# Kernel tuning notes

Hardware: AMD Instinct MI355X
Metric: run time of the kernel (lower is better)

The kernel has to match this reference:

```python
import jax, jax.numpy as jnp
import numpy as np

B, T, F, H = 2048, 512, 64, 16


def setup_inputs() -> dict:
    key = jax.random.key(0)
    ks = jax.random.split(key, 10)
    s = 0.05  # small init so relu-activated LSTM state stays bounded over 512 steps
    return {
        "x": jax.random.normal(ks[0], (B, T, F), dtype=jnp.float32),
        "Wx": jax.random.normal(ks[1], (F, 4 * H), dtype=jnp.float32) * s,
        "Wh": jax.random.normal(ks[2], (H, 4 * H), dtype=jnp.float32) * s,
        "b": jnp.zeros((4 * H,), dtype=jnp.float32),
        "W2": jax.random.normal(ks[3], (H, 8), dtype=jnp.float32) * 0.3,
        "b2": jnp.zeros((8,), dtype=jnp.float32),
        "W3": jax.random.normal(ks[4], (8, 4), dtype=jnp.float32) * 0.3,
        "b3": jnp.zeros((4,), dtype=jnp.float32),
        "Wo": jax.random.normal(ks[5], (4, 1), dtype=jnp.float32) * 0.3,
        "bo": jnp.zeros((1,), dtype=jnp.float32),
    }


def reference(x, Wx, Wh, b, W2, b2, W3, b3, Wo, bo):
    # Keras LSTM, gate order [i, f, c(g), o]; recurrent_activation=sigmoid,
    # activation=relu (applied to candidate g AND to cell state in h = o*relu(c)).
    # Precompute input projections for all timesteps, scan only the recurrence.
    xz = jnp.einsum('btf,fg->btg', x, Wx) + b  # [B, T, 4H]
    h0 = jnp.zeros((x.shape[0], H), dtype=x.dtype)
    c0 = jnp.zeros((x.shape[0], H), dtype=x.dtype)

    def step(carry, xz_t):
        h, c = carry
        z = xz_t + h @ Wh  # [B, 4H]
        i = jax.nn.sigmoid(z[:, 0 * H:1 * H])
        f = jax.nn.sigmoid(z[:, 1 * H:2 * H])
        g = jax.nn.relu(z[:, 2 * H:3 * H])
        o = jax.nn.sigmoid(z[:, 3 * H:4 * H])
        c_new = f * c + i * g
        h_new = o * jax.nn.relu(c_new)
        return (h_new, c_new), None

    (h_T, _), _ = jax.lax.scan(step, (h0, c0), jnp.swapaxes(xz, 0, 1))
    # Dropout layers are identity at inference (training=False).
    x2 = jax.nn.relu(h_T @ W2 + b2)
    x3 = jax.nn.relu(x2 @ W3 + b3)
    return jax.nn.sigmoid(x3 @ Wo + bo)  # [B, 1]
```

## Files before the change

### kernel.cpp

```cpp
#include <hip/hip_runtime.h>
#include <stdint.h>

#define Bdim 2048
#define Tdim 512
#define NBLK (Tdim / 16)

#define TSTRIDE 68
#define BUFD (16 * TSTRIDE)

typedef __attribute__((ext_vector_type(8))) short bf16x8;
typedef __attribute__((ext_vector_type(4))) float f32x4;

__device__ __forceinline__ uint16_t f2bf(float f) {
    union { float f; uint32_t u; } v; v.f = f;
    uint32_t r = v.u + 0x7fffu + ((v.u >> 16) & 1u);
    return (uint16_t)(r >> 16);
}
__device__ __forceinline__ float sigmoidf(float z) {
    return __builtin_amdgcn_rcpf(1.0f + __expf(-z));
}

__global__ __launch_bounds__(64, 2) void lstm_fused(
    const float* __restrict__ x, const float* __restrict__ Wx,
    const float* __restrict__ bias, const float* __restrict__ Wh,
    const float* __restrict__ W2, const float* __restrict__ b2,
    const float* __restrict__ W3, const float* __restrict__ b3,
    const float* __restrict__ Wo, const float* __restrict__ bo,
    float* __restrict__ out)
{
    __shared__ __align__(16) float zbuf[2 * BUFD];
    __shared__ __align__(16) float hbuf[16];

    const int lane = threadIdx.x;
    const int l15  = lane & 15;
    const int quad = lane >> 4;
    const int b    = blockIdx.x;

    float w[16];
    #pragma unroll
    for (int k = 0; k < 16; ++k) w[k] = Wh[(size_t)k * 64 + lane];

    bf16x8 wxf[4][2];
    #pragma unroll
    for (int nt = 0; nt < 4; ++nt)
        #pragma unroll
        for (int kc = 0; kc < 2; ++kc)
            #pragma unroll
            for (int jj = 0; jj < 8; ++jj)
                wxf[nt][kc][jj] =
                    (short)f2bf(Wx[(size_t)(kc * 32 + quad * 8 + jj) * 64 + nt * 16 + l15]);

    float bv[4];
    #pragma unroll
    for (int nt = 0; nt < 4; ++nt) bv[nt] = bias[nt * 16 + l15];

    float4 xn[4];
    auto load_tile = [&](int t0) {
        const float* p = x + ((size_t)b * Tdim + t0 + l15) * 64 + quad * 8;
        xn[0] = *(const float4*)(p);
        xn[1] = *(const float4*)(p + 4);
        xn[2] = *(const float4*)(p + 32);
        xn[3] = *(const float4*)(p + 36);
    };

    auto project = [&](int q) {
        bf16x8 af[2];
        #pragma unroll
        for (int kc = 0; kc < 2; ++kc) {
            const float4 p0 = xn[kc * 2], p1 = xn[kc * 2 + 1];
            af[kc][0] = (short)f2bf(p0.x); af[kc][1] = (short)f2bf(p0.y);
            af[kc][2] = (short)f2bf(p0.z); af[kc][3] = (short)f2bf(p0.w);
            af[kc][4] = (short)f2bf(p1.x); af[kc][5] = (short)f2bf(p1.y);
            af[kc][6] = (short)f2bf(p1.z); af[kc][7] = (short)f2bf(p1.w);
        }
        f32x4 acc[4];
        #pragma unroll
        for (int nt = 0; nt < 4; ++nt) {
            f32x4 a = {bv[nt], bv[nt], bv[nt], bv[nt]};
            a = __builtin_amdgcn_mfma_f32_16x16x32_bf16(af[0], wxf[nt][0], a, 0, 0, 0);
            a = __builtin_amdgcn_mfma_f32_16x16x32_bf16(af[1], wxf[nt][1], a, 0, 0, 0);
            acc[nt] = a;
        }
        #pragma unroll
        for (int reg = 0; reg < 4; ++reg) {
            float4 w4;
            w4.x = acc[0][reg]; w4.y = acc[1][reg];
            w4.z = acc[2][reg]; w4.w = acc[3][reg];
            *(float4*)&zbuf[q * BUFD + (quad * 4 + reg) * TSTRIDE + l15 * 4] = w4;
        }
    };

    const int zoff = l15 * 4 + quad;
    auto readz = [&](int q, int t) -> float {
        return zbuf[q * BUFD + t * TSTRIDE + zoff];
    };

    load_tile(0);
    project(0);
    load_tile(16);

    float c = 0.f, h = 0.f;
    float hk[16];
    #pragma unroll
    for (int k = 0; k < 16; ++k) hk[k] = 0.f;
    float zc = readz(0, 0);

    for (int n = 0; n < NBLK; ++n) {
        const int p = n & 1;
        if (n + 1 < NBLK) {
            project(p ^ 1);
            if (n + 2 < NBLK) load_tile((n + 2) * 16);
        }
        #pragma unroll
        for (int u = 0; u < 16; ++u) {
            float zn = (u < 15) ? readz(p, u + 1) : readz(p ^ 1, 0);

            float a0 = zc, a1 = 0.f;
            #pragma unroll
            for (int k = 0; k < 8; ++k) {
                a0 = fmaf(hk[k],     w[k],     a0);
                a1 = fmaf(hk[k + 8], w[k + 8], a1);
            }
            const float z = a0 + a1;
            const float sig = sigmoidf(z);
            const float a = (quad == 2) ? fmaxf(z, 0.f) : sig;

            const float i_ = __shfl(a, l15);
            const float f_ = __shfl(a, l15 + 16);
            const float g_ = __shfl(a, l15 + 32);
            const float o_ = __shfl(a, l15 + 48);

            c = fmaf(f_, c, i_ * g_);
            h = o_ * fmaxf(c, 0.f);

            hbuf[l15] = h;
            const float4* hb = (const float4*)hbuf;
            float4 h0 = hb[0], h1 = hb[1], h2 = hb[2], h3 = hb[3];
            hk[0]  = h0.x; hk[1]  = h0.y; hk[2]  = h0.z; hk[3]  = h0.w;
            hk[4]  = h1.x; hk[5]  = h1.y; hk[6]  = h1.z; hk[7]  = h1.w;
            hk[8]  = h2.x; hk[9]  = h2.y; hk[10] = h2.z; hk[11] = h2.w;
            hk[12] = h3.x; hk[13] = h3.y; hk[14] = h3.z; hk[15] = h3.w;

            zc = zn;
        }
    }

    if (lane == 0) {
        float x2[8];
        #pragma unroll
        for (int k = 0; k < 8; ++k) {
            float s = b2[k];
            #pragma unroll
            for (int q = 0; q < 16; ++q) s = fmaf(hk[q], W2[(size_t)q * 8 + k], s);
            x2[k] = fmaxf(s, 0.f);
        }
        float x3[4];
        #pragma unroll
        for (int m = 0; m < 4; ++m) {
            float s = b3[m];
            #pragma unroll
            for (int k = 0; k < 8; ++k) s = fmaf(x2[k], W3[(size_t)k * 4 + m], s);
            x3[m] = fmaxf(s, 0.f);
        }
        float s = bo[0];
        #pragma unroll
        for (int m = 0; m < 4; ++m) s = fmaf(x3[m], Wo[m], s);
        out[b] = sigmoidf(s);
    }
}

extern "C" void kernel_launch(void* const* d_in, const int* in_sizes, int n_in,
                              void* d_out, int out_size, void* d_ws, size_t ws_size,
                              hipStream_t stream) {
    const float* x  = (const float*)d_in[0];
    const float* Wx = (const float*)d_in[1];
    const float* Wh = (const float*)d_in[2];
    const float* bb = (const float*)d_in[3];
    const float* W2 = (const float*)d_in[4];
    const float* b2 = (const float*)d_in[5];
    const float* W3 = (const float*)d_in[6];
    const float* b3 = (const float*)d_in[7];
    const float* Wo = (const float*)d_in[8];
    const float* bo = (const float*)d_in[9];

    lstm_fused<<<Bdim, 64, 0, stream>>>(x, Wx, bb, Wh, W2, b2, W3, b3,
                                        Wo, bo, (float*)d_out);
}
```

Baseline: 386.0 us.

## Batch 16 sequences per block with MFMA recurrence and warp-specialized projection

```diff
diff --git a/kernel.cpp b/kernel.cpp
--- a/kernel.cpp
+++ b/kernel.cpp
@@ -3,13 +3,19 @@
 
 #define Bdim 2048
 #define Tdim 512
-#define NBLK (Tdim / 16)
-
-#define TSTRIDE 68
-#define BUFD (16 * TSTRIDE)
+#define TT 8
+#define NT (Tdim / TT)
+
+#define XSTR (TT * 64 + 4)
+#define XBUF (16 * XSTR)
+#define ZSTR 68
+#define ZTS  (16 * ZSTR)
+#define ZBUF (TT * ZTS)
 
 typedef __attribute__((ext_vector_type(8))) short bf16x8;
 typedef __attribute__((ext_vector_type(4))) float f32x4;
+
+union U32x4 { uint32_t u[4]; bf16x8 v; };
 
 __device__ __forceinline__ uint16_t f2bf(float f) {
     union { float f; uint32_t u; } v; v.f = f;
@@ -19,8 +25,20 @@
 __device__ __forceinline__ float sigmoidf(float z) {
     return __builtin_amdgcn_rcpf(1.0f + __expf(-z));
 }
-
-__global__ __launch_bounds__(64, 2) void lstm_fused(
+__device__ __forceinline__ float fast_exp2(float x) {
+#if __has_builtin(__builtin_amdgcn_exp2f)
+    return __builtin_amdgcn_exp2f(x);
+#else
+    return exp2f(x);
+#endif
+}
+__device__ __forceinline__ void gld16(const float* gsrc, float* ldst) {
+    __builtin_amdgcn_global_load_lds(
+        (__attribute__((address_space(1))) void*)(gsrc),
+        (__attribute__((address_space(3))) void*)(ldst), 16, 0, 0);
+}
+
+__global__ __launch_bounds__(128, 1) void lstm_fused(
     const float* __restrict__ x, const float* __restrict__ Wx,
     const float* __restrict__ bias, const float* __restrict__ Wh,
     const float* __restrict__ W2, const float* __restrict__ b2,
@@ -28,144 +46,170 @@
     const float* __restrict__ Wo, const float* __restrict__ bo,
     float* __restrict__ out)
 {
-    __shared__ __align__(16) float zbuf[2 * BUFD];
-    __shared__ __align__(16) float hbuf[16];
-
-    const int lane = threadIdx.x;
-    const int l15  = lane & 15;
-    const int quad = lane >> 4;
-    const int b    = blockIdx.x;
-
-    float w[16];
-    #pragma unroll
-    for (int k = 0; k < 16; ++k) w[k] = Wh[(size_t)k * 64 + lane];
-
-    bf16x8 wxf[4][2];
-    #pragma unroll
-    for (int nt = 0; nt < 4; ++nt)
-        #pragma unroll
-        for (int kc = 0; kc < 2; ++kc)
-            #pragma unroll
-            for (int jj = 0; jj < 8; ++jj)
-                wxf[nt][kc][jj] =
-                    (short)f2bf(Wx[(size_t)(kc * 32 + quad * 8 + jj) * 64 + nt * 16 + l15]);
-
-    float bv[4];
-    #pragma unroll
-    for (int nt = 0; nt < 4; ++nt) bv[nt] = bias[nt * 16 + l15];
-
-    float4 xn[4];
-    auto load_tile = [&](int t0) {
-        const float* p = x + ((size_t)b * Tdim + t0 + l15) * 64 + quad * 8;
-        xn[0] = *(const float4*)(p);
-        xn[1] = *(const float4*)(p + 4);
-        xn[2] = *(const float4*)(p + 32);
-        xn[3] = *(const float4*)(p + 36);
+    __shared__ __align__(16) float xlds[2 * XBUF];
+    __shared__ __align__(16) float zbuf[2 * ZBUF];
+    __shared__ __align__(16) float hlds[16 * 17];
+
+    const int lane = threadIdx.x & 63;
+    const int wid  = threadIdx.x >> 6;
+    const int q = lane >> 4;
+    const int j = lane & 15;
+    const int b0 = blockIdx.x * 16;
+    const float KLOG2E = 1.4426950408889634f;
+
+    bf16x8 awx[4][2];
+    f32x4  bcol[4];
+    bf16x8 awh[4];
+    float  cst[4] = {0.f, 0.f, 0.f, 0.f};
+    float  hh[4]  = {0.f, 0.f, 0.f, 0.f};
+    uint32_t hw0 = 0, hw1 = 0;
+
+    auto gload = [&](int tile, int buf) {
+        const float* src0 = x + ((size_t)b0 * Tdim + tile * TT) * 64 + lane * 4;
+        #pragma unroll
+        for (int rb = 0; rb < 16; ++rb) {
+            const float* s = src0 + (size_t)rb * Tdim * 64;
+            float* d = &xlds[buf * XBUF + rb * XSTR];
+            gld16(s, d);
+            gld16(s + 256, d + 256);
+        }
     };
 
-    auto project = [&](int q) {
-        bf16x8 af[2];
-        #pragma unroll
-        for (int kc = 0; kc < 2; ++kc) {
-            const float4 p0 = xn[kc * 2], p1 = xn[kc * 2 + 1];
-            af[kc][0] = (short)f2bf(p0.x); af[kc][1] = (short)f2bf(p0.y);
-            af[kc][2] = (short)f2bf(p0.z); af[kc][3] = (short)f2bf(p0.w);
-            af[kc][4] = (short)f2bf(p1.x); af[kc][5] = (short)f2bf(p1.y);
-            af[kc][6] = (short)f2bf(p1.z); af[kc][7] = (short)f2bf(p1.w);
-        }
-        f32x4 acc[4];
+    auto proj = [&](int srcbuf, int dstbuf) {
+        const float* xb = &xlds[srcbuf * XBUF] + j * XSTR + q * 8;
+        float* zb = &zbuf[dstbuf * ZBUF] + j * ZSTR + q * 4;
+        #pragma unroll
+        for (int t = 0; t < TT; ++t) {
+            const float* px = xb + t * 64;
+            f32x4 x0 = *(const f32x4*)(px);
+            f32x4 x1 = *(const f32x4*)(px + 4);
+            f32x4 x2 = *(const f32x4*)(px + 32);
+            f32x4 x3 = *(const f32x4*)(px + 36);
+            U32x4 bx0, bx1;
+            asm("v_cvt_pk_bf16_f32 %0, %1, %2" : "=v"(bx0.u[0]) : "v"(x0[0]), "v"(x0[1]));
+            asm("v_cvt_pk_bf16_f32 %0, %1, %2" : "=v"(bx0.u[1]) : "v"(x0[2]), "v"(x0[3]));
+            asm("v_cvt_pk_bf16_f32 %0, %1, %2" : "=v"(bx0.u[2]) : "v"(x1[0]), "v"(x1[1]));
+            asm("v_cvt_pk_bf16_f32 %0, %1, %2" : "=v"(bx0.u[3]) : "v"(x1[2]), "v"(x1[3]));
+            asm("v_cvt_pk_bf16_f32 %0, %1, %2" : "=v"(bx1.u[0]) : "v"(x2[0]), "v"(x2[1]));
+            asm("v_cvt_pk_bf16_f32 %0, %1, %2" : "=v"(bx1.u[1]) : "v"(x2[2]), "v"(x2[3]));
+            asm("v_cvt_pk_bf16_f32 %0, %1, %2" : "=v"(bx1.u[2]) : "v"(x3[0]), "v"(x3[1]));
+            asm("v_cvt_pk_bf16_f32 %0, %1, %2" : "=v"(bx1.u[3]) : "v"(x3[2]), "v"(x3[3]));
+            #pragma unroll
+            for (int nt = 0; nt < 4; ++nt) {
+                f32x4 a = bcol[nt];
+                a = __builtin_amdgcn_mfma_f32_16x16x32_bf16(awx[nt][0], bx0.v, a, 0, 0, 0);
+                a = __builtin_amdgcn_mfma_f32_16x16x32_bf16(awx[nt][1], bx1.v, a, 0, 0, 0);
+                *(f32x4*)(zb + t * ZTS + nt * 16) = a;
+            }
+        }
+    };
+
+    if (wid == 1) {
         #pragma unroll
         for (int nt = 0; nt < 4; ++nt) {
-            f32x4 a = {bv[nt], bv[nt], bv[nt], bv[nt]};
-            a = __builtin_amdgcn_mfma_f32_16x16x32_bf16(af[0], wxf[nt][0], a, 0, 0, 0);
-            a = __builtin_amdgcn_mfma_f32_16x16x32_bf16(af[1], wxf[nt][1], a, 0, 0, 0);
-            acc[nt] = a;
-        }
-        #pragma unroll
-        for (int reg = 0; reg < 4; ++reg) {
-            float4 w4;
-            w4.x = acc[0][reg]; w4.y = acc[1][reg];
-            w4.z = acc[2][reg]; w4.w = acc[3][reg];
-            *(float4*)&zbuf[q * BUFD + (quad * 4 + reg) * TSTRIDE + l15 * 4] = w4;
-        }
-    };
-
-    const int zoff = l15 * 4 + quad;
-    auto readz = [&](int q, int t) -> float {
-        return zbuf[q * BUFD + t * TSTRIDE + zoff];
-    };
-
-    load_tile(0);
-    project(0);
-    load_tile(16);
-
-    float c = 0.f, h = 0.f;
-    float hk[16];
-    #pragma unroll
-    for (int k = 0; k < 16; ++k) hk[k] = 0.f;
-    float zc = readz(0, 0);
-
-    for (int n = 0; n < NBLK; ++n) {
-        const int p = n & 1;
-        if (n + 1 < NBLK) {
-            project(p ^ 1);
-            if (n + 2 < NBLK) load_tile((n + 2) * 16);
-        }
-        #pragma unroll
-        for (int u = 0; u < 16; ++u) {
-            float zn = (u < 15) ? readz(p, u + 1) : readz(p ^ 1, 0);
-
-            float a0 = zc, a1 = 0.f;
+            const float s = (nt == 2) ? 1.0f : -KLOG2E;
+            #pragma unroll
+            for (int kc = 0; kc < 2; ++kc)
+                #pragma unroll
+                for (int jj = 0; jj < 8; ++jj)
+                    awx[nt][kc][jj] = (short)f2bf(
+                        Wx[(size_t)(kc * 32 + q * 8 + jj) * 64 + nt * 16 + j] * s);
+            #pragma unroll
+            for (int r = 0; r < 4; ++r)
+                bcol[nt][r] = bias[nt * 16 + q * 4 + r] * s;
+        }
+        gload(0, 0);
+        asm volatile("s_waitcnt vmcnt(0)" ::: "memory");
+    } else {
+        #pragma unroll
+        for (int nt = 0; nt < 4; ++nt) {
+            const float s = (nt == 2) ? 1.0f : -KLOG2E;
+            bf16x8 a;
+            #pragma unroll
+            for (int e = 0; e < 8; ++e) a[e] = 0;
+            #pragma unroll
+            for (int e = 0; e < 4; ++e)
+                a[e] = (short)f2bf(Wh[(size_t)(q * 4 + e) * 64 + nt * 16 + j] * s);
+            awh[nt] = a;
+        }
+    }
+    __syncthreads();
+    if (wid == 1) {
+        gload(1, 1);
+        proj(0, 0);
+        asm volatile("s_waitcnt vmcnt(0) lgkmcnt(0)" ::: "memory");
+    }
+    __syncthreads();
+
+    for (int n = 0; n < NT; ++n) {
+        if (wid == 0) {
+            const float* zp = &zbuf[(n & 1) * ZBUF] + j * ZSTR + q * 4;
+            f32x4 zc0 = *(const f32x4*)(zp);
+            f32x4 zc1 = *(const f32x4*)(zp + 16);
+            f32x4 zc2 = *(const f32x4*)(zp + 32);
+            f32x4 zc3 = *(const f32x4*)(zp + 48);
+            #pragma unroll
+            for (int t = 0; t < TT; ++t) {
+                f32x4 zn0, zn1, zn2, zn3;
+                if (t < TT - 1) {
+                    const float* zq = zp + (t + 1) * ZTS;
+                    zn0 = *(const f32x4*)(zq);
+                    zn1 = *(const f32x4*)(zq + 16);
+                    zn2 = *(const f32x4*)(zq + 32);
+                    zn3 = *(const f32x4*)(zq + 48);
+                }
+                U32x4 hbu; hbu.u[0] = hw0; hbu.u[1] = hw1; hbu.u[2] = 0; hbu.u[3] = 0;
+                f32x4 ai = __builtin_amdgcn_mfma_f32_16x16x32_bf16(awh[0], hbu.v, zc0, 0, 0, 0);
+                f32x4 af = __builtin_amdgcn_mfma_f32_16x16x32_bf16(awh[1], hbu.v, zc1, 0, 0, 0);
+                f32x4 ag = __builtin_amdgcn_mfma_f32_16x16x32_bf16(awh[2], hbu.v, zc2, 0, 0, 0);
+                f32x4 ao = __builtin_amdgcn_mfma_f32_16x16x32_bf16(awh[3], hbu.v, zc3, 0, 0, 0);
+                #pragma unroll
+                for (int r = 0; r < 4; ++r) {
+                    float si = __builtin_amdgcn_rcpf(1.0f + fast_exp2(ai[r]));
+                    float sf = __builtin_amdgcn_rcpf(1.0f + fast_exp2(af[r]));
+                    float so = __builtin_amdgcn_rcpf(1.0f + fast_exp2(ao[r]));
+                    float gg = fmaxf(ag[r], 0.0f);
+                    cst[r] = fmaf(sf, cst[r], si * gg);
+                    hh[r] = so * fmaxf(cst[r], 0.0f);
+                }
+                asm("v_cvt_pk_bf16_f32 %0, %1, %2" : "=v"(hw0) : "v"(hh[0]), "v"(hh[1]));
+                asm("v_cvt_pk_bf16_f32 %0, %1, %2" : "=v"(hw1) : "v"(hh[2]), "v"(hh[3]));
+                if (t < TT - 1) { zc0 = zn0; zc1 = zn1; zc2 = zn2; zc3 = zn3; }
+            }
+        } else {
+            if (n + 2 < NT) gload(n + 2, n & 1);
+            if (n + 1 < NT) proj((n + 1) & 1, (n + 1) & 1);
+            asm volatile("s_waitcnt vmcnt(0) lgkmcnt(0)" ::: "memory");
+        }
+        __syncthreads();
+    }
+
+    if (wid == 0) {
+        #pragma unroll
+        for (int r = 0; r < 4; ++r) hlds[j * 17 + q * 4 + r] = hh[r];
+        if (lane < 16) {
+            const float* hp = &hlds[lane * 17];
+            float x2[8];
             #pragma unroll
             for (int k = 0; k < 8; ++k) {
-                a0 = fmaf(hk[k],     w[k],     a0);
-                a1 = fmaf(hk[k + 8], w[k + 8], a1);
-            }
-            const float z = a0 + a1;
-            const float sig = sigmoidf(z);
-            const float a = (quad == 2) ? fmaxf(z, 0.f) : sig;
-
-            const float i_ = __shfl(a, l15);
-            const float f_ = __shfl(a, l15 + 16);
-            const float g_ = __shfl(a, l15 + 32);
-            const float o_ = __shfl(a, l15 + 48);
-
-            c = fmaf(f_, c, i_ * g_);
-            h = o_ * fmaxf(c, 0.f);
-
-            hbuf[l15] = h;
-            const float4* hb = (const float4*)hbuf;
-            float4 h0 = hb[0], h1 = hb[1], h2 = hb[2], h3 = hb[3];
-            hk[0]  = h0.x; hk[1]  = h0.y; hk[2]  = h0.z; hk[3]  = h0.w;
-            hk[4]  = h1.x; hk[5]  = h1.y; hk[6]  = h1.z; hk[7]  = h1.w;
-            hk[8]  = h2.x; hk[9]  = h2.y; hk[10] = h2.z; hk[11] = h2.w;
-            hk[12] = h3.x; hk[13] = h3.y; hk[14] = h3.z; hk[15] = h3.w;
-
-            zc = zn;
-        }
-    }
-
-    if (lane == 0) {
-        float x2[8];
-        #pragma unroll
-        for (int k = 0; k < 8; ++k) {
-            float s = b2[k];
-            #pragma unroll
-            for (int q = 0; q < 16; ++q) s = fmaf(hk[q], W2[(size_t)q * 8 + k], s);
-            x2[k] = fmaxf(s, 0.f);
-        }
-        float x3[4];
-        #pragma unroll
-        for (int m = 0; m < 4; ++m) {
-            float s = b3[m];
-            #pragma unroll
-            for (int k = 0; k < 8; ++k) s = fmaf(x2[k], W3[(size_t)k * 4 + m], s);
-            x3[m] = fmaxf(s, 0.f);
-        }
-        float s = bo[0];
-        #pragma unroll
-        for (int m = 0; m < 4; ++m) s = fmaf(x3[m], Wo[m], s);
-        out[b] = sigmoidf(s);
+                float s = b2[k];
+                #pragma unroll
+                for (int u = 0; u < 16; ++u) s = fmaf(hp[u], W2[(size_t)u * 8 + k], s);
+                x2[k] = fmaxf(s, 0.f);
+            }
+            float x3[4];
+            #pragma unroll
+            for (int m = 0; m < 4; ++m) {
+                float s = b3[m];
+                #pragma unroll
+                for (int k = 0; k < 8; ++k) s = fmaf(x2[k], W3[(size_t)k * 4 + m], s);
+                x3[m] = fmaxf(s, 0.f);
+            }
+            float s = bo[0];
+            #pragma unroll
+            for (int m = 0; m < 4; ++m) s = fmaf(x3[m], Wo[m], s);
+            out[b0 + lane] = sigmoidf(s);
+        }
     }
 }
 
@@ -183,6 +227,6 @@
     const float* Wo = (const float*)d_in[8];
     const float* bo = (const float*)d_in[9];
 
-    lstm_fused<<<Bdim, 64, 0, stream>>>(x, Wx, bb, Wh, W2, b2, W3, b3,
-                                        Wo, bo, (float*)d_out);
-}
+    lstm_fused<<<Bdim / 16, 128, 0, stream>>>(x, Wx, bb, Wh, W2, b2, W3, b3,
+                                              Wo, bo, (float*)d_out);
+}
```

New measurement: 452.7 us. 1.17x slower.
